# Kernel tuning notes

Hardware: AMD Instinct MI355X
Metric: run time of the kernel (lower is better)

## Reference

```python
import jax, jax.numpy as jnp
import numpy as np

NUM_HEADS = 16
HEAD_DIM = 128
ROPE_BASE = 10000.0


def _rotate_half(x):
    x1, x2 = jnp.split(x, 2, axis=-1)
    return jnp.concatenate([-x2, x1], axis=-1)


def setup_inputs() -> dict:
    key = jax.random.key(0)
    ks = jax.random.split(key, 6)
    B, S, H = 2, 2048, 2048
    hidden_states = jax.random.normal(ks[0], (B, S, H), dtype=jnp.float32)
    # causal additive mask: 0 on/below diagonal, large negative above
    causal = jnp.tril(jnp.ones((S, S), dtype=bool))
    attention_mask = jnp.where(causal, 0.0, -1e9).astype(jnp.float32)[None, None]
    position_ids = jnp.broadcast_to(jnp.arange(S, dtype=jnp.int64), (B, S))
    sc = 1.0 / np.sqrt(H)
    Wq = jax.random.normal(ks[1], (H, H), dtype=jnp.float32) * sc
    Wk = jax.random.normal(ks[2], (H, H), dtype=jnp.float32) * sc
    Wv = jax.random.normal(ks[3], (H, H), dtype=jnp.float32) * sc
    Wo = jax.random.normal(ks[4], (H, H), dtype=jnp.float32) * sc
    return {"hidden_states": hidden_states, "attention_mask": attention_mask,
            "position_ids": position_ids, "Wq": Wq, "Wk": Wk, "Wv": Wv, "Wo": Wo}


def reference(hidden_states, attention_mask, position_ids, Wq, Wk, Wv, Wo):
    B, S, H = hidden_states.shape
    nH, hd = NUM_HEADS, HEAD_DIM
    # projections (torch Linear: x @ W.T)
    q = (hidden_states @ Wq.T).reshape(B, S, nH, hd).transpose(0, 2, 1, 3)  # [B,nH,S,hd]
    k = (hidden_states @ Wk.T).reshape(B, S, nH, hd).transpose(0, 2, 1, 3)
    v = (hidden_states @ Wv.T).reshape(B, S, nH, hd).transpose(0, 2, 1, 3)
    # rotary embeddings: cos/sin cache over positions, duplicated to full head_dim
    inv_freq = 1.0 / (ROPE_BASE ** (jnp.arange(0, hd, 2, dtype=jnp.float32) / hd))  # [hd/2]
    t = jnp.arange(S, dtype=jnp.float32)
    freqs = jnp.outer(t, inv_freq)                       # [S, hd/2]
    emb = jnp.concatenate([freqs, freqs], axis=-1)       # [S, hd]
    cos = jnp.cos(emb)[position_ids][:, None]            # [B,1,S,hd]
    sin = jnp.sin(emb)[position_ids][:, None]
    q = q * cos + _rotate_half(q) * sin
    k = k * cos + _rotate_half(k) * sin
    # eager attention
    scores = jnp.einsum('bhqd,bhkd->bhqk', q, k) / np.sqrt(hd).astype(np.float32)
    scores = scores + attention_mask
    attn = jax.nn.softmax(scores, axis=-1)
    out = jnp.einsum('bhqk,bhkd->bhqd', attn, v)         # [B,nH,S,hd]
    out = out.transpose(0, 2, 1, 3).reshape(B, S, H)
    return out @ Wo.T
```

## Files before the change

### kernel.cpp

```cpp
#include <hip/hip_runtime.h>
#include <cstdint>
#include <cstddef>

#define NH    16
#define HD    128
#define SEQ   2048
#define HID   2048
#define BATCH 2
#define MTOT  (BATCH*SEQ)

#define SCALE 0.08838834764831845f
#define L2E   1.4426950408889634f
#define KSCL  (0.08838834764831845f * 1.4426950408889634f)
#define L2_10K_D64 0.20762050593046458f

typedef __bf16 bf16x8 __attribute__((ext_vector_type(8)));
typedef float  floatx4 __attribute__((ext_vector_type(4)));

__device__ __forceinline__ unsigned short f2bf(float f) {
  union { float f; unsigned u; } v; v.f = f;
  unsigned u = v.u;
  return (unsigned short)((u + 0x7FFFu + ((u >> 16) & 1u)) >> 16);
}
__device__ __forceinline__ float bf2f(unsigned short h) {
  union { unsigned u; float f; } v; v.u = ((unsigned)h) << 16; return v.f;
}

__device__ __forceinline__ void gld16(const unsigned short* g, unsigned short* l) {
  auto gp = reinterpret_cast<const __attribute__((address_space(1))) void*>(
      reinterpret_cast<uintptr_t>(g));
  auto lp = reinterpret_cast<__attribute__((address_space(3))) void*>(
      reinterpret_cast<uintptr_t>(l));
  __builtin_amdgcn_global_load_lds(gp, lp, 16, 0, 0);
}

__global__ void rope_tab(float2* __restrict__ T) {
  int idx = blockIdx.x * blockDim.x + threadIdx.x;
  int s = idx >> 6, i = idx & 63;
  float freq = exp2f(-(float)i * L2_10K_D64);
  float th = (float)s * freq;
  T[idx] = make_float2(cosf(th), sinf(th));
}

__global__ void cvt_all(const float* __restrict__ X,
                        const float* __restrict__ Wq, const float* __restrict__ Wk,
                        const float* __restrict__ Wv, const float* __restrict__ Wo,
                        unsigned short* __restrict__ Xb,
                        unsigned short* __restrict__ Wqb, unsigned short* __restrict__ Wkb,
                        unsigned short* __restrict__ Wvb, unsigned short* __restrict__ Wob) {
  int i = blockIdx.x * blockDim.x + threadIdx.x;
  const float* src; unsigned short* dst; int k;
  if (i < (1 << 21)) { src = X; dst = Xb; k = i; }
  else {
    int j = i - (1 << 21);
    int seg = j >> 20; k = j & ((1 << 20) - 1);
    src = (seg == 0) ? Wq : (seg == 1) ? Wk : (seg == 2) ? Wv : Wo;
    dst = (seg == 0) ? Wqb : (seg == 1) ? Wkb : (seg == 2) ? Wvb : Wob;
  }
  float4 v = reinterpret_cast<const float4*>(src)[k];
  ushort4 o;
  o.x = f2bf(v.x); o.y = f2bf(v.y); o.z = f2bf(v.z); o.w = f2bf(v.w);
  reinterpret_cast<ushort4*>(dst)[k] = o;
}


#define SBAR      asm volatile("s_barrier" ::: "memory")
#define WAITLGKM  asm volatile("s_waitcnt lgkmcnt(0)" ::: "memory")
#define WAITVM(n) asm volatile("s_waitcnt vmcnt(" #n ")" ::: "memory")
#define PRIO1     __builtin_amdgcn_s_setprio(1)
#define PRIO0     __builtin_amdgcn_s_setprio(0)
#define SCHED0    __builtin_amdgcn_sched_barrier(0)

#define STAGE_A(buf, half, t8)                                                  \
  {                                                                             \
    int row_ = tid >> 3;                                                        \
    int cgs_ = (tid & 7) ^ (row_ & 7);                                          \
    gld16(Ag + (size_t)((half) * 64 + row_) * HID + (t8) * 64 + cgs_ * 8,       \
          As + (buf) * 8192 + (half) * 4096 + tid * 8);                         \
  }

#define STAGE_B(buf, half, t8)                                                  \
  {                                                                             \
    _Pragma("unroll")                                                           \
    for (int j_ = 0; j_ < 2; ++j_) {                                            \
      int G_   = j_ * 512 + tid;                                                \
      int row_ = G_ >> 3;                                                       \
      int cgs_ = (G_ & 7) ^ (row_ & 7);                                         \
      gld16(Bg + (size_t)((half) * 128 + row_) * HID + (t8) * 64 + cgs_ * 8,    \
            Bs + (buf) * 16384 + (half) * 8192 + G_ * 8);                       \
    }                                                                           \
  }

#define LDA(buf, qm)                                                            \
  _Pragma("unroll")                                                             \
  for (int mr_ = 0; mr_ < 2; ++mr_)                                             \
    _Pragma("unroll")                                                           \
    for (int ks_ = 0; ks_ < 2; ++ks_)                                           \
      af[mr_][ks_] = *reinterpret_cast<const bf16x8*>(                          \
          &As[(buf) * 8192 + (wm * 64 + (qm) * 32 + mr_ * 16 + l16) * 64 + cgo[ks_]]);

#define LDB2(buf, nr0)                                                          \
  _Pragma("unroll")                                                             \
  for (int nr_ = 0; nr_ < 2; ++nr_)                                             \
    _Pragma("unroll")                                                           \
    for (int ks_ = 0; ks_ < 2; ++ks_)                                           \
      bfr[(nr0) + nr_][ks_] = *reinterpret_cast<const bf16x8*>(                 \
          &Bs[(buf) * 16384 + (((nr0) + nr_) * 64 + wn * 16 + l16) * 64 + cgo[ks_]]);

#define MM(qm, qn)                                                              \
  _Pragma("unroll")                                                             \
  for (int ks_ = 0; ks_ < 2; ++ks_)                                             \
    _Pragma("unroll")                                                           \
    for (int mr_ = 0; mr_ < 2; ++mr_)                                           \
      _Pragma("unroll")                                                         \
      for (int nr_ = 0; nr_ < 2; ++nr_)                                         \
        acc[(qm) * 2 + mr_][(qn) * 2 + nr_] =                                   \
            __builtin_amdgcn_mfma_f32_16x16x32_bf16(                            \
                af[mr_][ks_], bfr[(qn) * 2 + nr_][ks_],                         \
                acc[(qm) * 2 + mr_][(qn) * 2 + nr_], 0, 0, 0);

__global__ __launch_bounds__(512, 2)
void gemm_qkv128(const unsigned short* __restrict__ Xb,
                 const unsigned short* __restrict__ Wq,
                 const unsigned short* __restrict__ Wk,
                 const unsigned short* __restrict__ Wv,
                 const float2* __restrict__ ropeT,
                 unsigned short* __restrict__ Qo,
                 unsigned short* __restrict__ Ko,
                 unsigned short* __restrict__ Vto) {
  __shared__ unsigned short As[2 * 8192];
  __shared__ unsigned short Bs[2 * 16384];

  const int bid = blockIdx.x;
  const int xcd = bid & 7;
  const int j   = bid >> 3;
  const int zn  = xcd * 3 + (j >> 5);
  const int by  = j & 31;
  const int z   = zn >> 3;
  const int bx  = zn & 7;

  const unsigned short* W = (z == 0) ? Wq : (z == 1) ? Wk : Wv;
  const int mBase = by * 128, nBase = bx * 256;
  const unsigned short* Ag = Xb + (size_t)mBase * HID;
  const unsigned short* Bg = W  + (size_t)nBase * HID;

  const int tid  = threadIdx.x;
  const int wave = tid >> 6, lane = tid & 63;
  const int l16  = lane & 15, quad = lane >> 4;
  const int wm   = wave >> 2, wn = wave & 3;
  const int xr   = l16 & 7;
  const int cgo[2] = { ((quad) ^ xr) * 8, ((quad + 4) ^ xr) * 8 };

  floatx4 acc[4][4];
#pragma unroll
  for (int i = 0; i < 4; ++i)
#pragma unroll
    for (int jj = 0; jj < 4; ++jj) acc[i][jj] = {0.f, 0.f, 0.f, 0.f};

  bf16x8 af[2][2], bfr[4][2];

  STAGE_B(0, 0, 0); STAGE_B(0, 1, 0);
  STAGE_A(0, 0, 0); STAGE_A(0, 1, 0);
  STAGE_B(1, 0, 1); STAGE_B(1, 1, 1);
  WAITVM(4);
  SBAR;

#pragma unroll 1
  for (int i = 0; i < 15; ++i) {
    const int t = 2 * i;
    LDA(0, 0); LDB2(0, 0);
    STAGE_A(1, 0, t + 1);
    SBAR; WAITLGKM; SCHED0; PRIO1; MM(0, 0); PRIO0; SBAR;
    LDB2(0, 2);
    STAGE_A(1, 1, t + 1);
    SBAR; WAITLGKM; SCHED0; PRIO1; MM(0, 1); PRIO0; SBAR;
    LDA(0, 1);
    STAGE_B(0, 0, t + 2);
    SBAR; WAITLGKM; SCHED0; PRIO1; MM(1, 0); PRIO0; SBAR;
    STAGE_B(0, 1, t + 2);
    SBAR; SCHED0; PRIO1; MM(1, 1); PRIO0; WAITVM(4); SBAR;
    LDA(1, 0); LDB2(1, 0);
    STAGE_A(0, 0, t + 2);
    SBAR; WAITLGKM; SCHED0; PRIO1; MM(0, 0); PRIO0; SBAR;
    LDB2(1, 2);
    STAGE_A(0, 1, t + 2);
    SBAR; WAITLGKM; SCHED0; PRIO1; MM(0, 1); PRIO0; SBAR;
    LDA(1, 1);
    STAGE_B(1, 0, t + 3);
    SBAR; WAITLGKM; SCHED0; PRIO1; MM(1, 0); PRIO0; SBAR;
    STAGE_B(1, 1, t + 3);
    SBAR; SCHED0; PRIO1; MM(1, 1); PRIO0; WAITVM(4); SBAR;
  }

  LDA(0, 0); LDB2(0, 0);
  STAGE_A(1, 0, 31);
  SBAR; WAITLGKM; SCHED0; PRIO1; MM(0, 0); PRIO0; SBAR;
  LDB2(0, 2);
  STAGE_A(1, 1, 31);
  SBAR; WAITLGKM; SCHED0; PRIO1; MM(0, 1); PRIO0; SBAR;
  LDA(0, 1);
  SBAR; WAITLGKM; SCHED0; PRIO1; MM(1, 0); PRIO0; SBAR;
  SBAR; SCHED0; PRIO1; MM(1, 1); PRIO0; WAITVM(0); SBAR;
  LDA(1, 0); LDB2(1, 0);
  SBAR; WAITLGKM; SCHED0; PRIO1; MM(0, 0); PRIO0; SBAR;
  LDB2(1, 2);
  SBAR; WAITLGKM; SCHED0; PRIO1; MM(0, 1); PRIO0; SBAR;
  LDA(1, 1);
  SBAR; WAITLGKM; SCHED0; PRIO1; MM(1, 0); MM(1, 1); PRIO0;

  if (z < 2) {
    unsigned short* dst = (z == 0) ? Qo : Ko;
    const int hh0 = nBase >> 7;
    const int d1  = wn * 16 + l16;
#pragma unroll
    for (int mr = 0; mr < 4; ++mr) {
      int srow = mBase + wm * 64 + mr * 16 + quad * 4;
      int bb = srow >> 11, s = srow & (SEQ - 1);
#pragma unroll
      for (int r = 0; r < 4; ++r) {
        float2 cs = ropeT[(size_t)(s + r) * 64 + d1];
#pragma unroll
        for (int p = 0; p < 2; ++p) {
          float x1 = acc[mr][2 * p][r], x2 = acc[mr][2 * p + 1][r];
          size_t base = (((size_t)bb * NH + hh0 + p) * SEQ + (s + r)) * HD;
          dst[base + d1]      = f2bf(x1 * cs.x - x2 * cs.y);
          dst[base + d1 + 64] = f2bf(x2 * cs.x + x1 * cs.y);
        }
      }
    }
  } else {
#pragma unroll
    for (int mr = 0; mr < 4; ++mr) {
      int mrow = mBase + wm * 64 + mr * 16 + quad * 4;
      int bb = mrow >> 11, s = mrow & (SEQ - 1);
#pragma unroll
      for (int nr = 0; nr < 4; ++nr) {
        int n = nBase + nr * 64 + wn * 16 + l16;
        int hh = n >> 7, d = n & 127;
        ushort4 pk;
        pk.x = f2bf(acc[mr][nr][0]); pk.y = f2bf(acc[mr][nr][1]);
        pk.z = f2bf(acc[mr][nr][2]); pk.w = f2bf(acc[mr][nr][3]);
        *reinterpret_cast<ushort4*>(&Vto[(((size_t)bb * NH + hh) * HD + d) * SEQ + s]) = pk;
      }
    }
  }
}

__device__ __forceinline__ void gemm_core(const unsigned short* __restrict__ A,
                                          const unsigned short* __restrict__ B,
                                          int K, int mBase, int nBase,
                                          unsigned short* As, unsigned short* Bs,
                                          floatx4 acc[4][4]) {
  int tid  = threadIdx.x;
  int wave = tid >> 6, lane = tid & 63;
  int l16  = lane & 15, quad = lane >> 4;
  int wm   = wave >> 1, wn = wave & 1;

  const unsigned short* Ag = A + (size_t)mBase * K;
  const unsigned short* Bg = B + (size_t)nBase * K;

  for (int k0 = 0; k0 < K; k0 += 32) {
    __syncthreads();
#pragma unroll
    for (int r = 0; r < 2; ++r) {
      int row0 = wave * 32 + r * 16;
      int grow = row0 + (lane >> 2);
      int gcol = k0 + (lane & 3) * 8;
      gld16(Ag + (size_t)grow * K + gcol, As + row0 * 32 + lane * 8);
      gld16(Bg + (size_t)grow * K + gcol, Bs + row0 * 32 + lane * 8);
    }
    __syncthreads();

    bf16x8 af[4], bfr[4];
#pragma unroll
    for (int t = 0; t < 4; ++t) {
      af[t]  = *reinterpret_cast<const bf16x8*>(&As[(wm * 64 + t * 16 + l16) * 32 + quad * 8]);
      bfr[t] = *reinterpret_cast<const bf16x8*>(&Bs[(wn * 64 + t * 16 + l16) * 32 + quad * 8]);
    }
#pragma unroll
    for (int tm = 0; tm < 4; ++tm)
#pragma unroll
      for (int tn = 0; tn < 4; ++tn)
        acc[tm][tn] = __builtin_amdgcn_mfma_f32_16x16x32_bf16(af[tm], bfr[tn], acc[tm][tn], 0, 0, 0);
  }
}

__global__ __launch_bounds__(256)
void gemm_out(const unsigned short* __restrict__ Ob,
              const unsigned short* __restrict__ Wo,
              float* __restrict__ out) {
  __shared__ unsigned short As[128 * 32];
  __shared__ unsigned short Bs[128 * 32];
  int mBase = blockIdx.y * 128, nBase = blockIdx.x * 128;

  floatx4 acc[4][4];
#pragma unroll
  for (int i = 0; i < 4; ++i)
#pragma unroll
    for (int j = 0; j < 4; ++j) acc[i][j] = {0.f, 0.f, 0.f, 0.f};

  gemm_core(Ob, Wo, HID, mBase, nBase, As, Bs, acc);

  int tid = threadIdx.x;
  int wave = tid >> 6, lane = tid & 63;
  int l16 = lane & 15, quad = lane >> 4;
  int wm = wave >> 1, wn = wave & 1;

#pragma unroll
  for (int tm = 0; tm < 4; ++tm) {
    int mrow = mBase + wm * 64 + tm * 16 + quad * 4;
#pragma unroll
    for (int tn = 0; tn < 4; ++tn) {
      int n = nBase + wn * 64 + tn * 16 + l16;
#pragma unroll
      for (int r = 0; r < 4; ++r)
        out[(size_t)(mrow + r) * HID + n] = acc[tm][tn][r];
    }
  }
}

__global__ __launch_bounds__(512)
void attn_kernel(const unsigned short* __restrict__ Q,
                 const unsigned short* __restrict__ K,
                 const unsigned short* __restrict__ Vt,
                 unsigned short* __restrict__ Ob) {
  __shared__ unsigned short Ks[32 * 136];
  __shared__ unsigned short Vs[128 * 40];
  __shared__ unsigned short Ps[8][16 * 40];

  int qt = 15 - blockIdx.y;
  int bh = blockIdx.x;
  int b = bh >> 4, h = bh & 15;
  int q0 = qt * 128;
  int tid = threadIdx.x;
  int wave = tid >> 6, lane = tid & 63;
  int l16 = lane & 15, quad = lane >> 4;

  const size_t headQ = (size_t)bh * SEQ * HD;
  const size_t headV = (size_t)bh * HD * SEQ;

  bf16x8 qf[4];
  {
    int qrow = q0 + wave * 16 + l16;
    const unsigned short* qp = Q + headQ + (size_t)qrow * HD + quad * 8;
#pragma unroll
    for (int c = 0; c < 4; ++c)
      qf[c] = *reinterpret_cast<const bf16x8*>(qp + c * 32);
  }

  floatx4 oacc[8];
#pragma unroll
  for (int i = 0; i < 8; ++i) oacc[i] = {0.f, 0.f, 0.f, 0.f};
  float rs[4];
#pragma unroll
  for (int r = 0; r < 4; ++r) rs[r] = 0.f;

  int qq = q0 + wave * 16 + quad * 4;
  int qmax = q0 + wave * 16 + 15;
  unsigned short* pw = Ps[wave];

  int nkt = q0 / 32 + 4;
  for (int kt = 0; kt < nkt; ++kt) {
    int k0 = kt * 32;
    __syncthreads();
    {
      int row = tid >> 4, dc = (tid & 15) * 8;
      *reinterpret_cast<uint4*>(&Ks[row * 136 + dc]) =
        *reinterpret_cast<const uint4*>(&K[headQ + (size_t)(k0 + row) * HD + dc]);
    }
    {
      int row = tid >> 2, kc = (tid & 3) * 8;
      *reinterpret_cast<uint4*>(&Vs[row * 40 + kc]) =
        *reinterpret_cast<const uint4*>(&Vt[headV + (size_t)row * SEQ + k0 + kc]);
    }
    __syncthreads();

    if (k0 <= qmax) {
      floatx4 sc[2];
#pragma unroll
      for (int nt = 0; nt < 2; ++nt) {
        floatx4 s4 = {0.f, 0.f, 0.f, 0.f};
#pragma unroll
        for (int c = 0; c < 4; ++c) {
          bf16x8 kf = *reinterpret_cast<const bf16x8*>(&Ks[(nt * 16 + l16) * 136 + c * 32 + quad * 8]);
          s4 = __builtin_amdgcn_mfma_f32_16x16x32_bf16(qf[c], kf, s4, 0, 0, 0);
        }
        sc[nt] = s4;
      }

#pragma unroll
      for (int nt = 0; nt < 2; ++nt) {
        int kk = k0 + nt * 16 + l16;
#pragma unroll
        for (int r = 0; r < 4; ++r) {
          float arg = (kk <= qq + r) ? fmaf(sc[nt][r], KSCL, -32.0f) : -1e9f;
          float p = exp2f(arg);
          rs[r] += p;
          pw[(quad * 4 + r) * 40 + nt * 16 + l16] = f2bf(p);
        }
      }
      __asm__ __volatile__("s_waitcnt lgkmcnt(0)" ::: "memory");
      bf16x8 pf = *reinterpret_cast<const bf16x8*>(&pw[l16 * 40 + quad * 8]);

#pragma unroll
      for (int dt = 0; dt < 8; ++dt) {
        bf16x8 vf = *reinterpret_cast<const bf16x8*>(&Vs[(dt * 16 + l16) * 40 + quad * 8]);
        oacc[dt] = __builtin_amdgcn_mfma_f32_16x16x32_bf16(pf, vf, oacc[dt], 0, 0, 0);
      }
    }
  }

#pragma unroll
  for (int off = 1; off < 16; off <<= 1)
#pragma unroll
    for (int r = 0; r < 4; ++r) rs[r] += __shfl_xor(rs[r], off, 16);

  float inv[4];
#pragma unroll
  for (int r = 0; r < 4; ++r) inv[r] = 1.0f / rs[r];
#pragma unroll
  for (int dt = 0; dt < 8; ++dt)
#pragma unroll
    for (int r = 0; r < 4; ++r) {
      int s = q0 + wave * 16 + quad * 4 + r;
      Ob[(((size_t)b * SEQ + s) * NH + h) * HD + dt * 16 + l16] = f2bf(oacc[dt][r] * inv[r]);
    }
}

extern "C" void kernel_launch(void* const* d_in, const int* in_sizes, int n_in,
                              void* d_out, int out_size, void* d_ws, size_t ws_size,
                              hipStream_t stream) {
  const float* X  = (const float*)d_in[0];
  const float* Wq = (const float*)d_in[3];
  const float* Wk = (const float*)d_in[4];
  const float* Wv = (const float*)d_in[5];
  const float* Wo = (const float*)d_in[6];

  char* w = (char*)d_ws;
  size_t off = 0;
  auto alloc = [&](size_t bytes) { char* p = w + off; off += (bytes + 255) & ~(size_t)255; return p; };

  unsigned short* Xb  = (unsigned short*)alloc((size_t)MTOT * HID * 2);
  unsigned short* Wqb = (unsigned short*)alloc((size_t)HID * HID * 2);
  unsigned short* Wkb = (unsigned short*)alloc((size_t)HID * HID * 2);
  unsigned short* Wvb = (unsigned short*)alloc((size_t)HID * HID * 2);
  unsigned short* Wob = (unsigned short*)alloc((size_t)HID * HID * 2);
  unsigned short* Qb  = (unsigned short*)alloc((size_t)BATCH * NH * SEQ * HD * 2);
  unsigned short* Kb  = (unsigned short*)alloc((size_t)BATCH * NH * SEQ * HD * 2);
  unsigned short* Vtb = (unsigned short*)alloc((size_t)BATCH * NH * HD * SEQ * 2);
  unsigned short* Obf = (unsigned short*)alloc((size_t)BATCH * SEQ * NH * HD * 2);
  float2*         ropeT = (float2*)alloc((size_t)SEQ * 64 * sizeof(float2));

  rope_tab<<<(SEQ * 64) / 256, 256, 0, stream>>>(ropeT);

  const int nAll4 = (MTOT * HID + 4 * HID * HID) / 4;
  cvt_all<<<nAll4 / 256, 256, 0, stream>>>(X, Wq, Wk, Wv, Wo, Xb, Wqb, Wkb, Wvb, Wob);

  gemm_qkv128<<<768, 512, 0, stream>>>(Xb, Wqb, Wkb, Wvb, ropeT, Qb, Kb, Vtb);

  attn_kernel<<<dim3(BATCH * NH, SEQ / 128), 512, 0, stream>>>(Qb, Kb, Vtb, Obf);

  gemm_out<<<dim3(HID / 128, MTOT / 128), 256, 0, stream>>>(Obf, Wob, (float*)d_out);
}
```

Measured before the change: 403.0 us.

## Shrink QKV GEMM K-tile to 32 and prefetch K/V tiles into registers

The QKV projection GEMM now stages K-slices of 32 instead of 64. That halves its LDS footprint, raises the launch-bounds occupancy target from 2 to 4 blocks, and simplifies the double-buffered pipeline to 64 steps with a 4-way swizzle. The attention kernel now loads the next K and V tile into registers while the current tile is stored to LDS and computed, hiding global latency. The trade-off is more barriers per unit of work in the GEMM and extra register pressure in attention.

Result: faster. 382.8 us (-5.0%).

```diff
diff --git a/kernel.cpp b/kernel.cpp
--- a/kernel.cpp
+++ b/kernel.cpp
@@ -71,65 +71,53 @@
 #define PRIO0     __builtin_amdgcn_s_setprio(0)
 #define SCHED0    __builtin_amdgcn_sched_barrier(0)
 
-#define STAGE_A(buf, half, t8)                                                  \
+#define STAGE_A(p, t8)                                                          \
   {                                                                             \
-    int row_ = tid >> 3;                                                        \
-    int cgs_ = (tid & 7) ^ (row_ & 7);                                          \
-    gld16(Ag + (size_t)((half) * 64 + row_) * HID + (t8) * 64 + cgs_ * 8,       \
-          As + (buf) * 8192 + (half) * 4096 + tid * 8);                         \
-  }
-
-#define STAGE_B(buf, half, t8)                                                  \
+    int row_ = tid >> 2, g_ = tid & 3;                                          \
+    gld16(Ag + (size_t)row_ * HID + (t8) * 32 + ((g_ ^ (row_ & 3)) * 8),        \
+          As + (p) * 4096 + tid * 8);                                           \
+  }
+
+#define STAGE_B(p, t8)                                                          \
   {                                                                             \
     _Pragma("unroll")                                                           \
     for (int j_ = 0; j_ < 2; ++j_) {                                            \
-      int G_   = j_ * 512 + tid;                                                \
-      int row_ = G_ >> 3;                                                       \
-      int cgs_ = (G_ & 7) ^ (row_ & 7);                                         \
-      gld16(Bg + (size_t)((half) * 128 + row_) * HID + (t8) * 64 + cgs_ * 8,    \
-            Bs + (buf) * 16384 + (half) * 8192 + G_ * 8);                       \
+      int G_ = j_ * 512 + tid;                                                  \
+      int row_ = G_ >> 2, g_ = G_ & 3;                                          \
+      gld16(Bg + (size_t)row_ * HID + (t8) * 32 + ((g_ ^ (row_ & 3)) * 8),      \
+            Bs + (p) * 8192 + G_ * 8);                                          \
     }                                                                           \
   }
 
-#define LDA(buf, qm)                                                            \
+#define READS(p)                                                                \
   _Pragma("unroll")                                                             \
-  for (int mr_ = 0; mr_ < 2; ++mr_)                                             \
+  for (int mr_ = 0; mr_ < 4; ++mr_)                                             \
+    af[mr_] = *reinterpret_cast<const bf16x8*>(                                 \
+        &As[(p) * 4096 + (wm * 64 + mr_ * 16 + l16) * 32 + cg]);                \
+  _Pragma("unroll")                                                             \
+  for (int nr_ = 0; nr_ < 4; ++nr_)                                             \
+    bfr[nr_] = *reinterpret_cast<const bf16x8*>(                                \
+        &Bs[(p) * 8192 + (nr_ * 64 + wn * 16 + l16) * 32 + cg]);
+
+#define MMH(h)                                                                  \
+  _Pragma("unroll")                                                             \
+  for (int mr_ = 0; mr_ < 4; ++mr_)                                             \
     _Pragma("unroll")                                                           \
-    for (int ks_ = 0; ks_ < 2; ++ks_)                                           \
-      af[mr_][ks_] = *reinterpret_cast<const bf16x8*>(                          \
-          &As[(buf) * 8192 + (wm * 64 + (qm) * 32 + mr_ * 16 + l16) * 64 + cgo[ks_]]);
-
-#define LDB2(buf, nr0)                                                          \
-  _Pragma("unroll")                                                             \
-  for (int nr_ = 0; nr_ < 2; ++nr_)                                             \
-    _Pragma("unroll")                                                           \
-    for (int ks_ = 0; ks_ < 2; ++ks_)                                           \
-      bfr[(nr0) + nr_][ks_] = *reinterpret_cast<const bf16x8*>(                 \
-          &Bs[(buf) * 16384 + (((nr0) + nr_) * 64 + wn * 16 + l16) * 64 + cgo[ks_]]);
-
-#define MM(qm, qn)                                                              \
-  _Pragma("unroll")                                                             \
-  for (int ks_ = 0; ks_ < 2; ++ks_)                                             \
-    _Pragma("unroll")                                                           \
-    for (int mr_ = 0; mr_ < 2; ++mr_)                                           \
-      _Pragma("unroll")                                                         \
-      for (int nr_ = 0; nr_ < 2; ++nr_)                                         \
-        acc[(qm) * 2 + mr_][(qn) * 2 + nr_] =                                   \
-            __builtin_amdgcn_mfma_f32_16x16x32_bf16(                            \
-                af[mr_][ks_], bfr[(qn) * 2 + nr_][ks_],                         \
-                acc[(qm) * 2 + mr_][(qn) * 2 + nr_], 0, 0, 0);
-
-__global__ __launch_bounds__(512, 2)
-void gemm_qkv128(const unsigned short* __restrict__ Xb,
-                 const unsigned short* __restrict__ Wq,
-                 const unsigned short* __restrict__ Wk,
-                 const unsigned short* __restrict__ Wv,
-                 const float2* __restrict__ ropeT,
-                 unsigned short* __restrict__ Qo,
-                 unsigned short* __restrict__ Ko,
-                 unsigned short* __restrict__ Vto) {
-  __shared__ unsigned short As[2 * 8192];
-  __shared__ unsigned short Bs[2 * 16384];
+    for (int nr_ = 0; nr_ < 2; ++nr_)                                           \
+      acc[mr_][(h) * 2 + nr_] = __builtin_amdgcn_mfma_f32_16x16x32_bf16(        \
+          af[mr_], bfr[(h) * 2 + nr_], acc[mr_][(h) * 2 + nr_], 0, 0, 0);
+
+__global__ __launch_bounds__(512, 4)
+void gemm_qkv32(const unsigned short* __restrict__ Xb,
+                const unsigned short* __restrict__ Wq,
+                const unsigned short* __restrict__ Wk,
+                const unsigned short* __restrict__ Wv,
+                const float2* __restrict__ ropeT,
+                unsigned short* __restrict__ Qo,
+                unsigned short* __restrict__ Ko,
+                unsigned short* __restrict__ Vto) {
+  __shared__ unsigned short As[2 * 4096];
+  __shared__ unsigned short Bs[2 * 8192];
 
   const int bid = blockIdx.x;
   const int xcd = bid & 7;
@@ -148,8 +136,7 @@
   const int wave = tid >> 6, lane = tid & 63;
   const int l16  = lane & 15, quad = lane >> 4;
   const int wm   = wave >> 2, wn = wave & 3;
-  const int xr   = l16 & 7;
-  const int cgo[2] = { ((quad) ^ xr) * 8, ((quad + 4) ^ xr) * 8 };
+  const int cg   = (quad ^ (l16 & 3)) * 8;
 
   floatx4 acc[4][4];
 #pragma unroll
@@ -157,56 +144,30 @@
 #pragma unroll
     for (int jj = 0; jj < 4; ++jj) acc[i][jj] = {0.f, 0.f, 0.f, 0.f};
 
-  bf16x8 af[2][2], bfr[4][2];
-
-  STAGE_B(0, 0, 0); STAGE_B(0, 1, 0);
-  STAGE_A(0, 0, 0); STAGE_A(0, 1, 0);
-  STAGE_B(1, 0, 1); STAGE_B(1, 1, 1);
-  WAITVM(4);
+  bf16x8 af[4], bfr[4];
+
+  STAGE_A(0, 0); STAGE_B(0, 0);
+  STAGE_A(1, 1); STAGE_B(1, 1);
+  WAITVM(3);
   SBAR;
 
 #pragma unroll 1
-  for (int i = 0; i < 15; ++i) {
+  for (int i = 0; i < 31; ++i) {
     const int t = 2 * i;
-    LDA(0, 0); LDB2(0, 0);
-    STAGE_A(1, 0, t + 1);
-    SBAR; WAITLGKM; SCHED0; PRIO1; MM(0, 0); PRIO0; SBAR;
-    LDB2(0, 2);
-    STAGE_A(1, 1, t + 1);
-    SBAR; WAITLGKM; SCHED0; PRIO1; MM(0, 1); PRIO0; SBAR;
-    LDA(0, 1);
-    STAGE_B(0, 0, t + 2);
-    SBAR; WAITLGKM; SCHED0; PRIO1; MM(1, 0); PRIO0; SBAR;
-    STAGE_B(0, 1, t + 2);
-    SBAR; SCHED0; PRIO1; MM(1, 1); PRIO0; WAITVM(4); SBAR;
-    LDA(1, 0); LDB2(1, 0);
-    STAGE_A(0, 0, t + 2);
-    SBAR; WAITLGKM; SCHED0; PRIO1; MM(0, 0); PRIO0; SBAR;
-    LDB2(1, 2);
-    STAGE_A(0, 1, t + 2);
-    SBAR; WAITLGKM; SCHED0; PRIO1; MM(0, 1); PRIO0; SBAR;
-    LDA(1, 1);
-    STAGE_B(1, 0, t + 3);
-    SBAR; WAITLGKM; SCHED0; PRIO1; MM(1, 0); PRIO0; SBAR;
-    STAGE_B(1, 1, t + 3);
-    SBAR; SCHED0; PRIO1; MM(1, 1); PRIO0; WAITVM(4); SBAR;
-  }
-
-  LDA(0, 0); LDB2(0, 0);
-  STAGE_A(1, 0, 31);
-  SBAR; WAITLGKM; SCHED0; PRIO1; MM(0, 0); PRIO0; SBAR;
-  LDB2(0, 2);
-  STAGE_A(1, 1, 31);
-  SBAR; WAITLGKM; SCHED0; PRIO1; MM(0, 1); PRIO0; SBAR;
-  LDA(0, 1);
-  SBAR; WAITLGKM; SCHED0; PRIO1; MM(1, 0); PRIO0; SBAR;
-  SBAR; SCHED0; PRIO1; MM(1, 1); PRIO0; WAITVM(0); SBAR;
-  LDA(1, 0); LDB2(1, 0);
-  SBAR; WAITLGKM; SCHED0; PRIO1; MM(0, 0); PRIO0; SBAR;
-  LDB2(1, 2);
-  SBAR; WAITLGKM; SCHED0; PRIO1; MM(0, 1); PRIO0; SBAR;
-  LDA(1, 1);
-  SBAR; WAITLGKM; SCHED0; PRIO1; MM(1, 0); MM(1, 1); PRIO0;
+    READS(0);
+    WAITLGKM; SCHED0; PRIO1; MMH(0); PRIO0; SBAR;
+    STAGE_A(0, t + 2); STAGE_B(0, t + 2);
+    SCHED0; PRIO1; MMH(1); PRIO0; WAITVM(3); SBAR;
+    READS(1);
+    WAITLGKM; SCHED0; PRIO1; MMH(0); PRIO0; SBAR;
+    STAGE_A(1, t + 3); STAGE_B(1, t + 3);
+    SCHED0; PRIO1; MMH(1); PRIO0; WAITVM(3); SBAR;
+  }
+  READS(0);
+  WAITLGKM; SCHED0; PRIO1; MMH(0); PRIO0; SBAR;
+  SCHED0; PRIO1; MMH(1); PRIO0; WAITVM(0); SBAR;
+  READS(1);
+  WAITLGKM; SCHED0; PRIO1; MMH(0); MMH(1); PRIO0;
 
   if (z < 2) {
     unsigned short* dst = (z == 0) ? Qo : Ko;
@@ -359,20 +320,22 @@
   int qmax = q0 + wave * 16 + 15;
   unsigned short* pw = Ps[wave];
 
+  const int krow = tid >> 4, kdc = (tid & 15) * 8;
+  const int vrow = tid >> 2, vkc = (tid & 3) * 8;
+
   int nkt = q0 / 32 + 4;
+
+  uint4 kreg = *reinterpret_cast<const uint4*>(&K[headQ + (size_t)krow * HD + kdc]);
+  uint4 vreg = *reinterpret_cast<const uint4*>(&Vt[headV + (size_t)vrow * SEQ + vkc]);
+
   for (int kt = 0; kt < nkt; ++kt) {
     int k0 = kt * 32;
     __syncthreads();
-    {
-      int row = tid >> 4, dc = (tid & 15) * 8;
-      *reinterpret_cast<uint4*>(&Ks[row * 136 + dc]) =
-        *reinterpret_cast<const uint4*>(&K[headQ + (size_t)(k0 + row) * HD + dc]);
-    }
-    {
-      int row = tid >> 2, kc = (tid & 3) * 8;
-      *reinterpret_cast<uint4*>(&Vs[row * 40 + kc]) =
-        *reinterpret_cast<const uint4*>(&Vt[headV + (size_t)row * SEQ + k0 + kc]);
-    }
+    *reinterpret_cast<uint4*>(&Ks[krow * 136 + kdc]) = kreg;
+    *reinterpret_cast<uint4*>(&Vs[vrow * 40 + vkc]) = vreg;
+    int k0n = (kt + 1 < nkt) ? (k0 + 32) : k0;
+    kreg = *reinterpret_cast<const uint4*>(&K[headQ + (size_t)(k0n + krow) * HD + kdc]);
+    vreg = *reinterpret_cast<const uint4*>(&Vt[headV + (size_t)vrow * SEQ + k0n + vkc]);
     __syncthreads();
 
     if (k0 <= qmax) {
@@ -456,7 +419,7 @@
   const int nAll4 = (MTOT * HID + 4 * HID * HID) / 4;
   cvt_all<<<nAll4 / 256, 256, 0, stream>>>(X, Wq, Wk, Wv, Wo, Xb, Wqb, Wkb, Wvb, Wob);
 
-  gemm_qkv128<<<768, 512, 0, stream>>>(Xb, Wqb, Wkb, Wvb, ropeT, Qb, Kb, Vtb);
+  gemm_qkv32<<<768, 512, 0, stream>>>(Xb, Wqb, Wkb, Wvb, ropeT, Qb, Kb, Vtb);
 
   attn_kernel<<<dim3(BATCH * NH, SEQ / 128), 512, 0, stream>>>(Qb, Kb, Vtb, Obf);
 
```
